# Kernel optimization log

Hardware: AMD Instinct MI355X
Metric: run time of the kernel (lower is better)

## Reference

```python
import jax, jax.numpy as jnp
import numpy as np

B, S, D, H = 2, 2048, 1024, 16
DK = D // H


def setup_inputs() -> dict:
    key = jax.random.key(0)
    ks = jax.random.split(key, 12)
    scale = 1.0 / np.sqrt(D)
    inp = {
        "query": jax.random.normal(ks[0], (B, S, D), jnp.float32),
        "key_in": jax.random.normal(ks[1], (B, S, D), jnp.float32),
        "value": jax.random.normal(ks[2], (B, S, D), jnp.float32),
        "mask": jnp.ones((1, 1, S, S), dtype=bool),
        "w_q": jax.random.normal(ks[3], (D, D), jnp.float32) * scale,
        "b_q": jnp.zeros((D,), jnp.float32),
        "w_k": jax.random.normal(ks[4], (D, D), jnp.float32) * scale,
        "b_k": jnp.zeros((D,), jnp.float32),
        "w_v": jax.random.normal(ks[5], (D, D), jnp.float32) * scale,
        "b_v": jnp.zeros((D,), jnp.float32),
        "w_o": jax.random.normal(ks[6], (D, D), jnp.float32) * scale,
        "b_o": jnp.zeros((D,), jnp.float32),
    }
    return inp


def reference(query, key_in, value, mask, w_q, b_q, w_k, b_k, w_v, b_v, w_o, b_o):
    # QKV projections (nn.Linear: x @ W.T + b; here weights stored as [D_in, D_out])
    q = query @ w_q + b_q          # [B, S, D]
    k = key_in @ w_k + b_k
    v = value @ w_v + b_v
    # split heads -> [B, H, S, DK]
    q = q.reshape(B, S, H, DK).transpose(0, 2, 1, 3)
    k = k.reshape(B, S, H, DK).transpose(0, 2, 1, 3)
    v = v.reshape(B, S, H, DK).transpose(0, 2, 1, 3)
    # scaled dot-product attention (naive: full [B,H,S,S] scores)
    scores = jnp.einsum('bhqd,bhkd->bhqk', q, k) / jnp.sqrt(jnp.float32(DK))
    scores = jnp.where(mask, scores, jnp.float32(-1e9))
    probs = jax.nn.softmax(scores, axis=-1)  # dropout p=0.0 -> identity
    x = jnp.einsum('bhqk,bhkd->bhqd', probs, v)  # [B, H, S, DK]
    x = x.transpose(0, 2, 1, 3).reshape(B, S, D)
    return x @ w_o + b_o
```

## Files before the change

kernel.cpp:

```cpp
#include <hip/hip_runtime.h>
#include <cstdint>
#include <cstddef>


typedef _Float16 f16_t;
typedef _Float16 f16x8 __attribute__((ext_vector_type(8)));
typedef _Float16 f16x4 __attribute__((ext_vector_type(4)));
typedef float    f32x4 __attribute__((ext_vector_type(4)));

#define S_LEN 2048
#define DMODEL 1024
#define NHEAD 16
#define DK 64

__device__ __forceinline__ void async_copy16(void* lds, const void* g) {
    __builtin_amdgcn_global_load_lds(
        (const __attribute__((address_space(1))) unsigned int*)g,
        (__attribute__((address_space(3))) unsigned int*)lds,
        16, 0, 0);
}

__device__ __forceinline__ float fexp2(float x) {
#if __has_builtin(__builtin_amdgcn_exp2f)
    return __builtin_amdgcn_exp2f(x);
#else
    return exp2f(x);
#endif
}

__global__ __launch_bounds__(256) void cvt3_kernel(
    const float* __restrict__ s0, const float* __restrict__ s1, const float* __restrict__ s2,
    f16_t* __restrict__ d0, f16_t* __restrict__ d1, f16_t* __restrict__ d2, int n)
{
    const float* s = blockIdx.y == 0 ? s0 : blockIdx.y == 1 ? s1 : s2;
    f16_t*       d = blockIdx.y == 0 ? d0 : blockIdx.y == 1 ? d1 : d2;
    int i = (blockIdx.x * 256 + threadIdx.x) * 4;
    if (i + 3 < n) {
        f32x4 v = *(const f32x4*)(s + i);
        f16x4 o;
        o[0] = (f16_t)v[0]; o[1] = (f16_t)v[1];
        o[2] = (f16_t)v[2]; o[3] = (f16_t)v[3];
        *(f16x4*)(d + i) = o;
    }
}

__global__ __launch_bounds__(256) void transpose_cvt_kernel(
    const float* __restrict__ w0, const float* __restrict__ w1,
    const float* __restrict__ w2, const float* __restrict__ w3,
    f16_t* __restrict__ wt_base)
{
    __shared__ float tile[32][33];
    int z = blockIdx.z;
    const float* w = z == 0 ? w0 : z == 1 ? w1 : z == 2 ? w2 : w3;
    f16_t* wt = wt_base + (size_t)z * DMODEL * DMODEL;
    int tx = threadIdx.x, ty = threadIdx.y;
    int bx = blockIdx.x * 32;
    int by = blockIdx.y * 32;
#pragma unroll
    for (int i = 0; i < 4; ++i)
        tile[ty + i * 8][tx] = w[(size_t)(bx + ty + i * 8) * DMODEL + by + tx];
    __syncthreads();
#pragma unroll
    for (int i = 0; i < 4; ++i)
        wt[(size_t)(by + ty + i * 8) * DMODEL + bx + tx] = (f16_t)tile[tx][ty + i * 8];
}

__global__ __launch_bounds__(256) void qkv_gemm_kernel(
    const f16_t* __restrict__ Aq, const f16_t* __restrict__ Ak, const f16_t* __restrict__ Av,
    const f16_t* __restrict__ Bt,
    const float* __restrict__ bq, const float* __restrict__ bk, const float* __restrict__ bv,
    f16_t* __restrict__ q_h, f16_t* __restrict__ k_h, f16_t* __restrict__ v_t)
{
    __shared__ f16_t As[128 * 32];
    __shared__ f16_t Bs[128 * 32];

    int tid  = threadIdx.x;
    int lane = tid & 63;
    int w    = tid >> 6;
    int wm   = w >> 1, wn = w & 1;
    int row0 = blockIdx.y * 128;
    int col0 = blockIdx.x * 128;
    int which = col0 >> 10;
    const f16_t* A = which == 0 ? Aq : which == 1 ? Ak : Av;
    const float* bias = which == 0 ? bq : which == 1 ? bk : bv;

    f32x4 acc[4][4] = {};

    for (int kk = 0; kk < 1024; kk += 32) {
        __syncthreads();
#pragma unroll
        for (int j = 0; j < 2; ++j) {
            int c = w * 2 + j;
            int r = c * 16 + (lane >> 2);
            int e = (lane & 3) * 8;
            async_copy16(&As[c * 512], A  + (size_t)(row0 + r) * 1024 + kk + e);
            async_copy16(&Bs[c * 512], Bt + (size_t)(col0 + r) * 1024 + kk + e);
        }
        __syncthreads();

        f16x8 a[4], b[4];
#pragma unroll
        for (int mi = 0; mi < 4; ++mi)
            a[mi] = *(const f16x8*)&As[(wm * 64 + mi * 16 + (lane & 15)) * 32 + (lane >> 4) * 8];
#pragma unroll
        for (int ni = 0; ni < 4; ++ni)
            b[ni] = *(const f16x8*)&Bs[(wn * 64 + ni * 16 + (lane & 15)) * 32 + (lane >> 4) * 8];
#pragma unroll
        for (int mi = 0; mi < 4; ++mi)
#pragma unroll
            for (int ni = 0; ni < 4; ++ni)
                acc[mi][ni] = __builtin_amdgcn_mfma_f32_16x16x32_f16(a[mi], b[ni], acc[mi][ni], 0, 0, 0);
    }

    const float QSCALE = 0.125f * 1.4426950408889634f;
#pragma unroll
    for (int mi = 0; mi < 4; ++mi) {
#pragma unroll
        for (int ni = 0; ni < 4; ++ni) {
#pragma unroll
            for (int r = 0; r < 4; ++r) {
                int grow = row0 + wm * 64 + mi * 16 + (lane >> 4) * 4 + r;
                int gcol = col0 + wn * 64 + ni * 16 + (lane & 15);
                int nc   = gcol & 1023;
                float v  = acc[mi][ni][r] + bias[nc];
                int bb = grow >> 11, ss = grow & 2047;
                int hh = nc >> 6,    dd = nc & 63;
                if (which == 0)
                    q_h[(((size_t)(bb * NHEAD + hh) * S_LEN + ss) << 6) + dd] = (f16_t)(v * QSCALE);
                else if (which == 1)
                    k_h[(((size_t)(bb * NHEAD + hh) * S_LEN + ss) << 6) + dd] = (f16_t)v;
                else
                    v_t[((size_t)(bb * NHEAD + hh) * DK + dd) * S_LEN + ss] = (f16_t)v;
            }
        }
    }
}

__global__ __launch_bounds__(256) void out_gemm_kernel(
    const f16_t* __restrict__ A, const f16_t* __restrict__ Bt,
    const float* __restrict__ bias, float* __restrict__ outp)
{
    __shared__ f16_t As[128 * 32];
    __shared__ f16_t Bs[128 * 32];

    int tid  = threadIdx.x;
    int lane = tid & 63;
    int w    = tid >> 6;
    int wm   = w >> 1, wn = w & 1;
    int row0 = blockIdx.y * 128;
    int col0 = blockIdx.x * 128;

    f32x4 acc[4][4] = {};

    for (int kk = 0; kk < 1024; kk += 32) {
        __syncthreads();
#pragma unroll
        for (int j = 0; j < 2; ++j) {
            int c = w * 2 + j;
            int r = c * 16 + (lane >> 2);
            int e = (lane & 3) * 8;
            async_copy16(&As[c * 512], A  + (size_t)(row0 + r) * 1024 + kk + e);
            async_copy16(&Bs[c * 512], Bt + (size_t)(col0 + r) * 1024 + kk + e);
        }
        __syncthreads();

        f16x8 a[4], b[4];
#pragma unroll
        for (int mi = 0; mi < 4; ++mi)
            a[mi] = *(const f16x8*)&As[(wm * 64 + mi * 16 + (lane & 15)) * 32 + (lane >> 4) * 8];
#pragma unroll
        for (int ni = 0; ni < 4; ++ni)
            b[ni] = *(const f16x8*)&Bs[(wn * 64 + ni * 16 + (lane & 15)) * 32 + (lane >> 4) * 8];
#pragma unroll
        for (int mi = 0; mi < 4; ++mi)
#pragma unroll
            for (int ni = 0; ni < 4; ++ni)
                acc[mi][ni] = __builtin_amdgcn_mfma_f32_16x16x32_f16(a[mi], b[ni], acc[mi][ni], 0, 0, 0);
    }

#pragma unroll
    for (int mi = 0; mi < 4; ++mi)
#pragma unroll
        for (int ni = 0; ni < 4; ++ni)
#pragma unroll
            for (int r = 0; r < 4; ++r) {
                int grow = row0 + wm * 64 + mi * 16 + (lane >> 4) * 4 + r;
                int gcol = col0 + wn * 64 + ni * 16 + (lane & 15);
                outp[(size_t)grow * 1024 + gcol] = acc[mi][ni][r] + bias[gcol];
            }
}

__global__ __launch_bounds__(256) void flash_kernel(
    const f16_t* __restrict__ Q, const f16_t* __restrict__ K,
    const f16_t* __restrict__ Vt, f16_t* __restrict__ Ao)
{
    __shared__ f16_t Kl[2][64 * 64];
    __shared__ f16_t Vl[2][64 * 64];
    __shared__ f16_t Pw[4][32 * 72];

    int tid  = threadIdx.x;
    int lane = tid & 63;
    int li   = lane & 15;
    int g    = lane >> 4;
    int w    = tid >> 6;
    int qt   = blockIdx.x;
    int bh   = blockIdx.y;
    const size_t hbase = (size_t)bh * S_LEN * DK;
    const f16_t* Qh = Q  + hbase;
    const f16_t* Kh = K  + hbase;
    const f16_t* Vh = Vt + hbase;

    int q0 = qt * 128 + w * 32;

    f16x8 aq[2][2];
#pragma unroll
    for (int qc = 0; qc < 2; ++qc)
#pragma unroll
        for (int kc = 0; kc < 2; ++kc)
            aq[qc][kc] = *(const f16x8*)(Qh + (size_t)(q0 + qc * 16 + li) * DK + kc * 32 + g * 8);

    f32x4 ot[2][4] = {};
    float mrun[2] = {-1e30f, -1e30f};
    float lrun[2] = {0.f, 0.f};

    auto stage = [&](int buf, int kt) {
#pragma unroll
        for (int j = 0; j < 2; ++j) {
            int r0  = w * 16 + j * 8;
            int row = r0 + (lane >> 3);
            int sl  = (lane & 7) ^ (row & 7);
            async_copy16(&Kl[buf][r0 * 64], Kh + (size_t)(kt * 64 + row) * 64 + sl * 8);
            async_copy16(&Vl[buf][r0 * 64], Vh + (size_t)row * S_LEN + kt * 64 + sl * 8);
        }
    };

    stage(0, 0);
    int cur = 0;

    for (int kt = 0; kt < S_LEN / 64; ++kt) {
        __syncthreads();
        if (kt + 1 < S_LEN / 64) stage(cur ^ 1, kt + 1);

        f32x4 s[4][2] = {};
        __builtin_amdgcn_s_setprio(1);
#pragma unroll
        for (int kc = 0; kc < 2; ++kc)
#pragma unroll
            for (int kn = 0; kn < 4; ++kn) {
                int row = kn * 16 + li;
                int sp  = (kc * 4 + g) ^ (row & 7);
                f16x8 ak = *(const f16x8*)&Kl[cur][row * 64 + sp * 8];
                s[kn][0] = __builtin_amdgcn_mfma_f32_16x16x32_f16(ak, aq[0][kc], s[kn][0], 0, 0, 0);
                s[kn][1] = __builtin_amdgcn_mfma_f32_16x16x32_f16(ak, aq[1][kc], s[kn][1], 0, 0, 0);
            }
        __builtin_amdgcn_s_setprio(0);

#pragma unroll
        for (int qc = 0; qc < 2; ++qc) {
            float mx = -1e30f;
#pragma unroll
            for (int kn = 0; kn < 4; ++kn)
#pragma unroll
                for (int r = 0; r < 4; ++r)
                    mx = fmaxf(mx, s[kn][qc][r]);
            mx = fmaxf(mx, __shfl_xor(mx, 16));
            mx = fmaxf(mx, __shfl_xor(mx, 32));
            float mn = fmaxf(mrun[qc], mx);
            float alpha = fexp2(mrun[qc] - mn);
            mrun[qc] = mn;
            float rs = 0.f;
#pragma unroll
            for (int kn = 0; kn < 4; ++kn) {
                f16x4 pv;
#pragma unroll
                for (int r = 0; r < 4; ++r) {
                    float p = fexp2(s[kn][qc][r] - mn);
                    rs += p;
                    pv[r] = (f16_t)p;
                }
                *(f16x4*)&Pw[w][(qc * 16 + li) * 72 + kn * 16 + g * 4] = pv;
            }
            rs += __shfl_xor(rs, 16);
            rs += __shfl_xor(rs, 32);
            lrun[qc] = lrun[qc] * alpha + rs;
#pragma unroll
            for (int nd = 0; nd < 4; ++nd)
#pragma unroll
                for (int r = 0; r < 4; ++r)
                    ot[qc][nd][r] *= alpha;
        }

        __builtin_amdgcn_s_setprio(1);
#pragma unroll
        for (int kc = 0; kc < 2; ++kc) {
            f16x8 bp0 = *(const f16x8*)&Pw[w][(0 * 16 + li) * 72 + kc * 32 + g * 8];
            f16x8 bp1 = *(const f16x8*)&Pw[w][(1 * 16 + li) * 72 + kc * 32 + g * 8];
#pragma unroll
            for (int nd = 0; nd < 4; ++nd) {
                int row = nd * 16 + li;
                int sp  = (kc * 4 + g) ^ (row & 7);
                f16x8 av = *(const f16x8*)&Vl[cur][row * 64 + sp * 8];
                ot[0][nd] = __builtin_amdgcn_mfma_f32_16x16x32_f16(av, bp0, ot[0][nd], 0, 0, 0);
                ot[1][nd] = __builtin_amdgcn_mfma_f32_16x16x32_f16(av, bp1, ot[1][nd], 0, 0, 0);
            }
        }
        __builtin_amdgcn_s_setprio(0);

        cur ^= 1;
    }

    int b = bh >> 4, h = bh & 15;
#pragma unroll
    for (int qc = 0; qc < 2; ++qc) {
        float inv = 1.0f / lrun[qc];
        int qrow = q0 + qc * 16 + li;
        size_t base = (size_t)(b * S_LEN + qrow) * DMODEL + h * 64;
#pragma unroll
        for (int nd = 0; nd < 4; ++nd) {
            f16x4 ov;
#pragma unroll
            for (int r = 0; r < 4; ++r)
                ov[r] = (f16_t)(ot[qc][nd][r] * inv);
            *(f16x4*)&((f16_t*)Ao)[base + nd * 16 + g * 4] = ov;
        }
    }
}

extern "C" void kernel_launch(void* const* d_in, const int* in_sizes, int n_in,
                              void* d_out, int out_size, void* d_ws, size_t ws_size,
                              hipStream_t stream)
{
    const float* query  = (const float*)d_in[0];
    const float* key_in = (const float*)d_in[1];
    const float* value  = (const float*)d_in[2];
    const float* w_q = (const float*)d_in[4];
    const float* b_q = (const float*)d_in[5];
    const float* w_k = (const float*)d_in[6];
    const float* b_k = (const float*)d_in[7];
    const float* w_v = (const float*)d_in[8];
    const float* b_v = (const float*)d_in[9];
    const float* w_o = (const float*)d_in[10];
    const float* b_o = (const float*)d_in[11];
    float* out = (float*)d_out;

    char* ws = (char*)d_ws;
    const size_t MB = 1024 * 1024;
    f16_t* x_q  = (f16_t*)(ws + 0 * MB);
    f16_t* x_k  = (f16_t*)(ws + 8 * MB);
    f16_t* x_v  = (f16_t*)(ws + 16 * MB);
    f16_t* wt   = (f16_t*)(ws + 24 * MB);
    f16_t* wt_o = (f16_t*)(ws + 30 * MB);
    f16_t* q_h  = (f16_t*)(ws + 32 * MB);
    f16_t* k_h  = (f16_t*)(ws + 40 * MB);
    f16_t* v_t  = (f16_t*)(ws + 48 * MB);
    f16_t* attn = (f16_t*)(ws + 56 * MB);

    const int n = 2 * S_LEN * DMODEL;

    cvt3_kernel<<<dim3(n / 1024, 3), 256, 0, stream>>>(query, key_in, value, x_q, x_k, x_v, n);
    transpose_cvt_kernel<<<dim3(32, 32, 4), dim3(32, 8), 0, stream>>>(w_q, w_k, w_v, w_o, wt);

    qkv_gemm_kernel<<<dim3(24, 32), 256, 0, stream>>>(
        x_q, x_k, x_v, wt, b_q, b_k, b_v, q_h, k_h, v_t);

    flash_kernel<<<dim3(S_LEN / 128, 32), 256, 0, stream>>>(q_h, k_h, v_t, attn);

    out_gemm_kernel<<<dim3(8, 32), 256, 0, stream>>>(attn, wt_o, b_o, out);
}
```

Measured before the change: 157.0 us.

## Halve flash query tile, add lazy softmax rescale, split K/V staging, swizzle grids

The flash kernel now gives each block 64 queries (16 per wave), so twice as many blocks run with fewer registers each. It skips rescaling the output and running sum unless the row max grows by more than a threshold. K stays double-buffered while V becomes single-buffered and is loaded in the same iteration, with an explicit vmcnt wait placed before the PV matmul. All three GEMM/attention grids get a blockIdx swizzle meant to improve L2 locality. Trade-offs: K and V are re-read more often, and V loads are exposed within each iteration.

```diff
diff --git a/kernel.cpp b/kernel.cpp
--- a/kernel.cpp
+++ b/kernel.cpp
@@ -12,6 +12,7 @@
 #define DMODEL 1024
 #define NHEAD 16
 #define DK 64
+#define NKV (S_LEN / 64)
 
 __device__ __forceinline__ void async_copy16(void* lds, const void* g) {
     __builtin_amdgcn_global_load_lds(
@@ -78,8 +79,12 @@
     int lane = tid & 63;
     int w    = tid >> 6;
     int wm   = w >> 1, wn = w & 1;
-    int row0 = blockIdx.y * 128;
-    int col0 = blockIdx.x * 128;
+
+    int lin = blockIdx.y * 24 + blockIdx.x;
+    int swz = (lin & 7) * 96 + (lin >> 3);
+    int bx  = swz % 24, by = swz / 24;
+    int row0 = by * 128;
+    int col0 = bx * 128;
     int which = col0 >> 10;
     const f16_t* A = which == 0 ? Aq : which == 1 ? Ak : Av;
     const float* bias = which == 0 ? bq : which == 1 ? bk : bv;
@@ -147,8 +152,11 @@
     int lane = tid & 63;
     int w    = tid >> 6;
     int wm   = w >> 1, wn = w & 1;
-    int row0 = blockIdx.y * 128;
-    int col0 = blockIdx.x * 128;
+
+    int lin = blockIdx.y * 8 + blockIdx.x;
+    int swz = (lin & 7) * 32 + (lin >> 3);
+    int row0 = (swz / 8) * 128;
+    int col0 = (swz % 8) * 128;
 
     f32x4 acc[4][4] = {};
 
@@ -195,53 +203,64 @@
     const f16_t* __restrict__ Vt, f16_t* __restrict__ Ao)
 {
     __shared__ f16_t Kl[2][64 * 64];
-    __shared__ f16_t Vl[2][64 * 64];
-    __shared__ f16_t Pw[4][32 * 72];
+    __shared__ f16_t Vl[64 * 64];
+    __shared__ f16_t Pw[4][16 * 72];
 
     int tid  = threadIdx.x;
     int lane = tid & 63;
     int li   = lane & 15;
     int g    = lane >> 4;
     int w    = tid >> 6;
-    int qt   = blockIdx.x;
-    int bh   = blockIdx.y;
+
+    int lin = blockIdx.y * 32 + blockIdx.x;
+    int swz = (lin & 7) * 128 + (lin >> 3);
+    int qt  = swz & 31;
+    int bh  = swz >> 5;
+
     const size_t hbase = (size_t)bh * S_LEN * DK;
     const f16_t* Qh = Q  + hbase;
     const f16_t* Kh = K  + hbase;
     const f16_t* Vh = Vt + hbase;
 
-    int q0 = qt * 128 + w * 32;
-
-    f16x8 aq[2][2];
-#pragma unroll
-    for (int qc = 0; qc < 2; ++qc)
-#pragma unroll
-        for (int kc = 0; kc < 2; ++kc)
-            aq[qc][kc] = *(const f16x8*)(Qh + (size_t)(q0 + qc * 16 + li) * DK + kc * 32 + g * 8);
-
-    f32x4 ot[2][4] = {};
-    float mrun[2] = {-1e30f, -1e30f};
-    float lrun[2] = {0.f, 0.f};
-
-    auto stage = [&](int buf, int kt) {
+    int q0 = qt * 64 + w * 16;
+
+    f16x8 aq[2];
+#pragma unroll
+    for (int kc = 0; kc < 2; ++kc)
+        aq[kc] = *(const f16x8*)(Qh + (size_t)(q0 + li) * DK + kc * 32 + g * 8);
+
+    f32x4 ot[4] = {};
+    float mrun = -1e30f;
+    float lrun = 0.f;
+
+    auto stageV = [&](int kt) {
+#pragma unroll
+        for (int j = 0; j < 2; ++j) {
+            int r0  = w * 16 + j * 8;
+            int row = r0 + (lane >> 3);
+            int sl  = (lane & 7) ^ (row & 7);
+            async_copy16(&Vl[r0 * 64], Vh + (size_t)row * S_LEN + kt * 64 + sl * 8);
+        }
+    };
+    auto stageK = [&](int buf, int kt) {
 #pragma unroll
         for (int j = 0; j < 2; ++j) {
             int r0  = w * 16 + j * 8;
             int row = r0 + (lane >> 3);
             int sl  = (lane & 7) ^ (row & 7);
             async_copy16(&Kl[buf][r0 * 64], Kh + (size_t)(kt * 64 + row) * 64 + sl * 8);
-            async_copy16(&Vl[buf][r0 * 64], Vh + (size_t)row * S_LEN + kt * 64 + sl * 8);
         }
     };
 
-    stage(0, 0);
+    stageK(0, 0);
     int cur = 0;
 
-    for (int kt = 0; kt < S_LEN / 64; ++kt) {
-        __syncthreads();
-        if (kt + 1 < S_LEN / 64) stage(cur ^ 1, kt + 1);
-
-        f32x4 s[4][2] = {};
+    for (int kt = 0; kt < NKV; ++kt) {
+        __syncthreads();
+        stageV(kt);
+        if (kt + 1 < NKV) stageK(cur ^ 1, kt + 1);
+
+        f32x4 s[4] = {};
         __builtin_amdgcn_s_setprio(1);
 #pragma unroll
         for (int kc = 0; kc < 2; ++kc)
@@ -250,58 +269,58 @@
                 int row = kn * 16 + li;
                 int sp  = (kc * 4 + g) ^ (row & 7);
                 f16x8 ak = *(const f16x8*)&Kl[cur][row * 64 + sp * 8];
-                s[kn][0] = __builtin_amdgcn_mfma_f32_16x16x32_f16(ak, aq[0][kc], s[kn][0], 0, 0, 0);
-                s[kn][1] = __builtin_amdgcn_mfma_f32_16x16x32_f16(ak, aq[1][kc], s[kn][1], 0, 0, 0);
+                s[kn] = __builtin_amdgcn_mfma_f32_16x16x32_f16(ak, aq[kc], s[kn], 0, 0, 0);
             }
         __builtin_amdgcn_s_setprio(0);
 
-#pragma unroll
-        for (int qc = 0; qc < 2; ++qc) {
-            float mx = -1e30f;
-#pragma unroll
-            for (int kn = 0; kn < 4; ++kn)
-#pragma unroll
-                for (int r = 0; r < 4; ++r)
-                    mx = fmaxf(mx, s[kn][qc][r]);
+        {
+            float mx = fmaxf(fmaxf(fmaxf(s[0][0], s[0][1]), fmaxf(s[0][2], s[0][3])),
+                             fmaxf(fmaxf(s[1][0], s[1][1]), fmaxf(s[1][2], s[1][3])));
+            mx = fmaxf(mx, fmaxf(fmaxf(fmaxf(s[2][0], s[2][1]), fmaxf(s[2][2], s[2][3])),
+                                 fmaxf(fmaxf(s[3][0], s[3][1]), fmaxf(s[3][2], s[3][3]))));
             mx = fmaxf(mx, __shfl_xor(mx, 16));
             mx = fmaxf(mx, __shfl_xor(mx, 32));
-            float mn = fmaxf(mrun[qc], mx);
-            float alpha = fexp2(mrun[qc] - mn);
-            mrun[qc] = mn;
+            if (!__all(mx - mrun <= 8.0f)) {
+                float mn = fmaxf(mrun, mx);
+                float alpha = fexp2(mrun - mn);
+                mrun = mn;
+                lrun *= alpha;
+#pragma unroll
+                for (int nd = 0; nd < 4; ++nd)
+#pragma unroll
+                    for (int r = 0; r < 4; ++r)
+                        ot[nd][r] *= alpha;
+            }
             float rs = 0.f;
 #pragma unroll
             for (int kn = 0; kn < 4; ++kn) {
                 f16x4 pv;
 #pragma unroll
                 for (int r = 0; r < 4; ++r) {
-                    float p = fexp2(s[kn][qc][r] - mn);
+                    float p = fexp2(s[kn][r] - mrun);
                     rs += p;
                     pv[r] = (f16_t)p;
                 }
-                *(f16x4*)&Pw[w][(qc * 16 + li) * 72 + kn * 16 + g * 4] = pv;
+                *(f16x4*)&Pw[w][li * 72 + kn * 16 + g * 4] = pv;
             }
             rs += __shfl_xor(rs, 16);
             rs += __shfl_xor(rs, 32);
-            lrun[qc] = lrun[qc] * alpha + rs;
-#pragma unroll
-            for (int nd = 0; nd < 4; ++nd)
-#pragma unroll
-                for (int r = 0; r < 4; ++r)
-                    ot[qc][nd][r] *= alpha;
-        }
+            lrun += rs;
+        }
+
+        if (kt + 1 < NKV) asm volatile("s_waitcnt vmcnt(2)" ::: "memory");
+        else              asm volatile("s_waitcnt vmcnt(0)" ::: "memory");
 
         __builtin_amdgcn_s_setprio(1);
 #pragma unroll
         for (int kc = 0; kc < 2; ++kc) {
-            f16x8 bp0 = *(const f16x8*)&Pw[w][(0 * 16 + li) * 72 + kc * 32 + g * 8];
-            f16x8 bp1 = *(const f16x8*)&Pw[w][(1 * 16 + li) * 72 + kc * 32 + g * 8];
+            f16x8 bp = *(const f16x8*)&Pw[w][li * 72 + kc * 32 + g * 8];
 #pragma unroll
             for (int nd = 0; nd < 4; ++nd) {
                 int row = nd * 16 + li;
                 int sp  = (kc * 4 + g) ^ (row & 7);
-                f16x8 av = *(const f16x8*)&Vl[cur][row * 64 + sp * 8];
-                ot[0][nd] = __builtin_amdgcn_mfma_f32_16x16x32_f16(av, bp0, ot[0][nd], 0, 0, 0);
-                ot[1][nd] = __builtin_amdgcn_mfma_f32_16x16x32_f16(av, bp1, ot[1][nd], 0, 0, 0);
+                f16x8 av = *(const f16x8*)&Vl[row * 64 + sp * 8];
+                ot[nd] = __builtin_amdgcn_mfma_f32_16x16x32_f16(av, bp, ot[nd], 0, 0, 0);
             }
         }
         __builtin_amdgcn_s_setprio(0);
@@ -310,18 +329,17 @@
     }
 
     int b = bh >> 4, h = bh & 15;
-#pragma unroll
-    for (int qc = 0; qc < 2; ++qc) {
-        float inv = 1.0f / lrun[qc];
-        int qrow = q0 + qc * 16 + li;
+    {
+        float inv = 1.0f / lrun;
+        int qrow = q0 + li;
         size_t base = (size_t)(b * S_LEN + qrow) * DMODEL + h * 64;
 #pragma unroll
         for (int nd = 0; nd < 4; ++nd) {
             f16x4 ov;
 #pragma unroll
             for (int r = 0; r < 4; ++r)
-                ov[r] = (f16_t)(ot[qc][nd][r] * inv);
-            *(f16x4*)&((f16_t*)Ao)[base + nd * 16 + g * 4] = ov;
+                ov[r] = (f16_t)(ot[nd][r] * inv);
+            *(f16x4*)&Ao[base + nd * 16 + g * 4] = ov;
         }
     }
 }
@@ -363,7 +381,7 @@
     qkv_gemm_kernel<<<dim3(24, 32), 256, 0, stream>>>(
         x_q, x_k, x_v, wt, b_q, b_k, b_v, q_h, k_h, v_t);
 
-    flash_kernel<<<dim3(S_LEN / 128, 32), 256, 0, stream>>>(q_h, k_h, v_t, attn);
+    flash_kernel<<<dim3(32, 32), 256, 0, stream>>>(q_h, k_h, v_t, attn);
 
     out_gemm_kernel<<<dim3(8, 32), 256, 0, stream>>>(attn, wt_o, b_o, out);
 }
```

After: 152.3 us. 1.03x faster.
